# Kernel optimization log

Hardware: AMD Instinct MI355X
Metric: run time of the kernel (lower is better)

Reference implementation:

```python
import jax, jax.numpy as jnp
import numpy as np

B, S, D, H = 2, 2048, 512, 8
HID = 512
DH = HID // H  # 64


def setup_inputs() -> dict:
    key = jax.random.key(0)
    ks = jax.random.split(key, 11)
    sc = 0.02
    return {
        "q": jax.random.normal(ks[0], (B, S, D), jnp.float32),
        "k": jax.random.normal(ks[1], (B, S, D), jnp.float32),
        "v": jax.random.normal(ks[2], (B, S, D), jnp.float32),
        "Wq": jax.random.normal(ks[3], (D, HID), jnp.float32) * sc,
        "bq": jnp.zeros((HID,), jnp.float32),
        "Wk": jax.random.normal(ks[4], (D, HID), jnp.float32) * sc,
        "bk": jnp.zeros((HID,), jnp.float32),
        "Wv": jax.random.normal(ks[5], (D, HID), jnp.float32) * sc,
        "bv": jnp.zeros((HID,), jnp.float32),
        "Wo": jax.random.normal(ks[6], (HID, D), jnp.float32) * sc,
        "bo": jnp.zeros((D,), jnp.float32),
    }


def reference(q, k, v, Wq, bq, Wk, bk, Wv, bv, Wo, bo):
    # Linear projections: [B,S,D] -> [B,S,HID]
    qp = q @ Wq + bq
    kp = k @ Wk + bk
    vp = v @ Wv + bv
    # Faithful to torch .view(B, -1, S, head_dim): raw reshape, NOT a
    # [B,S,H,d] transpose. Head i reads a contiguous block of the buffer.
    qh = qp.reshape(B, H, S, DH)
    kh = kp.reshape(B, H, S, DH)
    vh = vp.reshape(B, H, S, DH)
    # scores [B,H,S,S]; NOTE: original divides by sqrt(d) AFTER softmax.
    scores = jnp.einsum("bhsd,bhtd->bhst", qh, kh)
    attn = jax.nn.softmax(scores, axis=-1) / np.sqrt(DH).astype(np.float32)
    ctx = jnp.einsum("bhst,bhtd->bhsd", attn, vh)
    # torch.cat over heads along last dim -> [B,S,H*d] with head blocks
    concat = jnp.transpose(ctx, (0, 2, 1, 3)).reshape(B, S, HID)
    return concat @ Wo + bo
```

## Files before the change

### kernel.cpp

```cpp
#include <hip/hip_runtime.h>
#include <hip/hip_bf16.h>

typedef __bf16 bf16_t;
typedef __bf16 bf16x8 __attribute__((ext_vector_type(8)));
typedef __bf16 bf16x4 __attribute__((ext_vector_type(4)));
typedef short short4v __attribute__((ext_vector_type(4)));
typedef float f32x4 __attribute__((ext_vector_type(4)));

static_assert(sizeof(bf16x8) == 16, "bf16x8 must be 16B");

#define BB 2
#define SS 2048
#define DD 512
#define HH 8
#define DH 64
#define LOG2E 1.44269504088896f

__global__ void prep(const float* __restrict__ q, const float* __restrict__ k,
                     const float* __restrict__ v, const float* __restrict__ w0,
                     const float* __restrict__ w1, const float* __restrict__ w2,
                     const float* __restrict__ w3, bf16_t* __restrict__ qkvb,
                     bf16_t* __restrict__ wt, int n) {
  const int tid = threadIdx.x;
  if (blockIdx.z < 3) {
    const float* src = (blockIdx.z == 0) ? q : (blockIdx.z == 1) ? k : v;
    bf16_t* out = qkvb + (size_t)blockIdx.z * n;
    int i = (blockIdx.x * 256 + tid) * 8;
    if (i >= n) return;
    const float4* s4 = (const float4*)(src + i);
    float4 a = s4[0], b = s4[1];
    bf16x8 o;
    o[0] = (bf16_t)a.x; o[1] = (bf16_t)a.y; o[2] = (bf16_t)a.z; o[3] = (bf16_t)a.w;
    o[4] = (bf16_t)b.x; o[5] = (bf16_t)b.y; o[6] = (bf16_t)b.z; o[7] = (bf16_t)b.w;
    *(bf16x8*)(out + i) = o;
  } else {
    __shared__ float tile[32][33];
    const int x = blockIdx.x;
    const int wsel = x >> 8;
    const int nb = ((x >> 4) & 15) * 32, kb = (x & 15) * 32;
    const int tx = tid & 31, ty = tid >> 5;
    const float* W = (wsel == 0) ? w0 : (wsel == 1) ? w1 : (wsel == 2) ? w2 : w3;
    bf16_t* out = wt + (size_t)wsel * 512 * 512;
#pragma unroll
    for (int i = 0; i < 4; i++)
      tile[ty + i * 8][tx] = W[(size_t)(kb + ty + i * 8) * 512 + nb + tx];
    __syncthreads();
#pragma unroll
    for (int i = 0; i < 4; i++)
      out[(size_t)(nb + ty + i * 8) * 512 + kb + tx] = (bf16_t)tile[tx][ty + i * 8];
  }
}

template <int BM, int BN, int WM, int WN, typename OutT>
__global__ __launch_bounds__(256) void gemm2(
    const bf16_t* __restrict__ Abase, const bf16_t* __restrict__ Btbase,
    const float* __restrict__ bias0, const float* __restrict__ bias1,
    const float* __restrict__ bias2, OutT* __restrict__ Cbase,
    int M, int N, int K, long Az, long Bz, long Cz, float scale0) {
  static_assert(BM == 2 * WM && BN == 2 * WN, "2x2 wave grid");
  constexpr int FM = WM / 16, FN = WN / 16;
  constexpr int AJ = BM / 32, BJ = BN / 32;

  const bf16_t* A  = Abase + (size_t)blockIdx.z * Az;
  const bf16_t* Bt = Btbase + (size_t)blockIdx.z * Bz;
  const float* bias = (blockIdx.z == 0) ? bias0 : (blockIdx.z == 1) ? bias1 : bias2;
  OutT* C = Cbase + (size_t)blockIdx.z * Cz;
  const float osc = (blockIdx.z == 0) ? scale0 : 1.0f;

  __shared__ bf16_t As[2][BM * 64];
  __shared__ bf16_t Bs[2][BN * 64];

  const int tid = threadIdx.x, w = tid >> 6, l = tid & 63;
  const int bm = blockIdx.y, bn = blockIdx.x;
  const int wm0 = (w >> 1) * WM, wn0 = (w & 1) * WN;
  const int lr = l & 15, lg = l >> 4;

  f32x4 acc[FM][FN] = {};

  auto stage = [&](int buf, int kt) {
#pragma unroll
    for (int j = 0; j < AJ; j++) {
      int lin = j * 256 + tid;
      int row = lin >> 3, cc = lin & 7;
      const bf16_t* g = A + (size_t)(bm * BM + row) * K + kt * 64 + cc * 8;
      __builtin_amdgcn_global_load_lds(
          (const __attribute__((address_space(1))) void*)g,
          (__attribute__((address_space(3))) void*)(&As[buf][(j * 256 + w * 64) * 8]), 16, 0, 0);
    }
#pragma unroll
    for (int j = 0; j < BJ; j++) {
      int lin = j * 256 + tid;
      int row = lin >> 3, cc = lin & 7;
      const bf16_t* g = Bt + (size_t)(bn * BN + row) * K + kt * 64 + cc * 8;
      __builtin_amdgcn_global_load_lds(
          (const __attribute__((address_space(1))) void*)g,
          (__attribute__((address_space(3))) void*)(&Bs[buf][(j * 256 + w * 64) * 8]), 16, 0, 0);
    }
  };

  stage(0, 0);
  const int KT = K >> 6;
  for (int kt = 0; kt < KT; kt++) {
    __syncthreads();
    if (kt + 1 < KT) stage((kt + 1) & 1, kt + 1);
    const bf16_t* as = As[kt & 1];
    const bf16_t* bs = Bs[kt & 1];
#pragma unroll
    for (int kc = 0; kc < 2; kc++) {
      bf16x8 a[FM], b[FN];
#pragma unroll
      for (int i = 0; i < FM; i++)
        a[i] = *(const bf16x8*)(as + (wm0 + i * 16 + lr) * 64 + kc * 32 + lg * 8);
#pragma unroll
      for (int j = 0; j < FN; j++)
        b[j] = *(const bf16x8*)(bs + (wn0 + j * 16 + lr) * 64 + kc * 32 + lg * 8);
#pragma unroll
      for (int i = 0; i < FM; i++)
#pragma unroll
        for (int j = 0; j < FN; j++)
          acc[i][j] = __builtin_amdgcn_mfma_f32_16x16x32_bf16(a[i], b[j], acc[i][j], 0, 0, 0);
    }
  }

  const int row0 = bm * BM + wm0, col0 = bn * BN + wn0;
#pragma unroll
  for (int j = 0; j < FN; j++) {
    int col = col0 + j * 16 + lr;
    float bv = bias[col];
#pragma unroll
    for (int i = 0; i < FM; i++) {
      int row = row0 + i * 16 + lg * 4;
#pragma unroll
      for (int r = 0; r < 4; r++) {
        float vv = (acc[i][j][r] + bv) * osc;
        C[(size_t)(row + r) * N + col] = (OutT)vv;
      }
    }
  }
}

__global__ __launch_bounds__(256, 8) void attn_flash(const bf16_t* __restrict__ qp,
                                                     const bf16_t* __restrict__ kp,
                                                     const bf16_t* __restrict__ vp,
                                                     bf16_t* __restrict__ Opart,
                                                     float* __restrict__ mlpart) {
  const int id = blockIdx.x;
  const int bh = (id & 7) | (((id >> 3) & 1) << 3);
  const int qt = (id >> 4) & 31;
  const int quarter = id >> 9;
  const int pidx = (((qt << 4) | bh) << 2) + quarter;

  const int tid = threadIdx.x, w = tid >> 6, l = tid & 63;
  const int lr = l & 15, lg = l >> 4;
  const size_t hb = (size_t)bh * (SS * DH);
  const bf16_t* Q = qp + hb;
  const bf16_t* Kh = kp + hb;
  const bf16_t* Vh = vp + hb;

  __shared__ __align__(16) bf16_t KsL[2][2048];
  __shared__ __align__(16) bf16_t VtL[2][2048];

  const int qr0 = qt * 64 + w * 16;

  bf16x8 aq[2];
#pragma unroll
  for (int kc = 0; kc < 2; kc++)
    aq[kc] = *(const bf16x8*)(Q + (size_t)(qr0 + lr) * DH + kc * 32 + lg * 8);

  f32x4 o[4] = {};
  float m_run = -1e30f, l_run = 0.f;

  const int krow = (w << 3) + (l >> 3);
  const int kcol = ((l & 7) ^ (l >> 3)) << 3;
  const bf16_t* ks_it = Kh + (size_t)(quarter * 16) * 2048 + krow * 64 + kcol;

  auto stage_k = [&](int buf, const bf16_t* ks) {
    char* kb = (char*)&KsL[buf][0];
    __builtin_amdgcn_global_load_lds((const __attribute__((address_space(1))) void*)ks,
        (__attribute__((address_space(3))) void*)(kb + (w << 10)), 16, 0, 0);
  };

  const int vkv = l & 31;
  const int vdv = (w << 1) | (l >> 5);
  bf16x8 vreg;
  auto load_v = [&](int it) {
    vreg = *(const bf16x8*)(Vh + ((size_t)it * 32 + vkv) * DH + vdv * 8);
  };
  auto write_v = [&](int buf) {
    char* vt = (char*)&VtL[buf][0];
#pragma unroll
    for (int j = 0; j < 8; j++) {
      int d = vdv * 8 + j;
      *(bf16_t*)(vt + d * 64 + ((vkv << 1) ^ (j << 3))) = vreg[j];
    }
  };

  const int it0 = quarter * 16;
  stage_k(0, ks_it);
  load_v(it0);
  write_v(0);

  for (int i = 0; i < 16; i++) {
    const int buf = i & 1;
    __syncthreads();
    if (i + 1 < 16) {
      ks_it += 2048;
      stage_k(buf ^ 1, ks_it);
      load_v(it0 + i + 1);
    }

    const char* ksb = (const char*)&KsL[buf][0];
    f32x4 s[2] = {};
    __builtin_amdgcn_s_setprio(1);
#pragma unroll
    for (int kc = 0; kc < 2; kc++) {
#pragma unroll
      for (int n = 0; n < 2; n++) {
        bf16x8 bk = *(const bf16x8*)(ksb + (n * 16 + lr) * 128 +
                                     ((kc * 64 + lg * 16) ^ ((lr & 7) << 4)));
        s[n] = __builtin_amdgcn_mfma_f32_16x16x32_bf16(bk, aq[kc], s[n], 0, 0, 0);
      }
    }
    __builtin_amdgcn_s_setprio(0);

    float pmax = -1e30f;
#pragma unroll
    for (int n = 0; n < 2; n++)
#pragma unroll
      for (int r = 0; r < 4; r++) pmax = fmaxf(pmax, s[n][r]);
    pmax = fmaxf(pmax, __shfl_xor(pmax, 16));
    pmax = fmaxf(pmax, __shfl_xor(pmax, 32));
    if (!__all(pmax <= m_run + 8.0f)) {
      float mnew = fmaxf(m_run, pmax);
      float scale = exp2f(m_run - mnew);
      l_run *= scale;
#pragma unroll
      for (int n = 0; n < 4; n++)
#pragma unroll
        for (int r = 0; r < 4; r++) o[n][r] *= scale;
      m_run = mnew;
    }
    float rs = 0.f;
#pragma unroll
    for (int n = 0; n < 2; n++)
#pragma unroll
      for (int r = 0; r < 4; r++) {
        float e = exp2f(s[n][r] - m_run);
        s[n][r] = e;
        rs += e;
      }
    l_run += rs;

    short4v pb[2];
#pragma unroll
    for (int c2 = 0; c2 < 2; c2++) {
      bf16x4 t;
#pragma unroll
      for (int r = 0; r < 4; r++) t[r] = (bf16_t)s[c2][r];
      pb[c2] = __builtin_bit_cast(short4v, t);
    }
    const char* vtb = (const char*)&VtL[buf][0];
    __builtin_amdgcn_s_setprio(1);
#pragma unroll
    for (int nd = 0; nd < 4; nd++) {
#pragma unroll
      for (int c2 = 0; c2 < 2; c2++) {
        bf16x4 bvh = *(const bf16x4*)(vtb + (nd * 16 + lr) * 64 +
                                      ((c2 * 32 + lg * 8) ^ ((lr & 7) << 3)));
        o[nd] = __builtin_amdgcn_mfma_f32_16x16x16bf16_1k(
            __builtin_bit_cast(short4v, bvh), pb[c2], o[nd], 0, 0, 0);
      }
    }
    __builtin_amdgcn_s_setprio(0);

    if (i + 1 < 16) write_v(buf ^ 1);
  }

  l_run += __shfl_xor(l_run, 16);
  l_run += __shfl_xor(l_run, 32);

  bf16_t* ob = Opart + (size_t)pidx * 4096;
#pragma unroll
  for (int n = 0; n < 4; n++) {
    bf16x4 t;
#pragma unroll
    for (int r = 0; r < 4; r++) t[r] = (bf16_t)o[n][r];
    *(bf16x4*)(ob + ((w * 4 + n) * 64 + l) * 4) = t;
  }
  if (lg == 0) {
    mlpart[(size_t)pidx * 128 + (w * 16 + lr) * 2 + 0] = m_run;
    mlpart[(size_t)pidx * 128 + (w * 16 + lr) * 2 + 1] = l_run;
  }
}

__global__ __launch_bounds__(256) void attn_combine(const bf16_t* __restrict__ Opart,
                                                    const float* __restrict__ mlpart,
                                                    bf16_t* __restrict__ ctx) {
  const int gid = blockIdx.x;
  const int qt = gid >> 4, bh = gid & 15;
  const int t = threadIdx.x, w = t >> 6, l = t & 63;
  const int lr = l & 15, lg = l >> 4;
  const int q = w * 16 + lr;

  float mv[4], lv[4];
#pragma unroll
  for (int s = 0; s < 4; s++) {
    const float* ml = mlpart + (size_t)(gid * 4 + s) * 128 + q * 2;
    mv[s] = ml[0];
    lv[s] = ml[1];
  }
  float m = fmaxf(fmaxf(mv[0], mv[1]), fmaxf(mv[2], mv[3]));
  float e[4], denom = 0.f;
#pragma unroll
  for (int s = 0; s < 4; s++) { e[s] = exp2f(mv[s] - m); denom += lv[s] * e[s]; }
  denom *= 8.0f;
  float f[4];
#pragma unroll
  for (int s = 0; s < 4; s++) f[s] = e[s] / denom;

  const int b = bh >> 3, h = bh & 7;
  const int trow = qt * 64 + q;
  size_t rowbase = ((size_t)b * SS + trow) * 512 + h * 64;

#pragma unroll
  for (int n = 0; n < 4; n++) {
    float acc[4] = {0.f, 0.f, 0.f, 0.f};
#pragma unroll
    for (int s = 0; s < 4; s++) {
      bf16x4 v = *(const bf16x4*)(Opart + (size_t)(gid * 4 + s) * 4096 +
                                  ((w * 4 + n) * 64 + l) * 4);
#pragma unroll
      for (int r = 0; r < 4; r++) acc[r] += (float)v[r] * f[s];
    }
    bf16x4 ov;
#pragma unroll
    for (int r = 0; r < 4; r++) ov[r] = (bf16_t)acc[r];
    *(bf16x4*)(&ctx[rowbase + n * 16 + lg * 4]) = ov;
  }
}

extern "C" void kernel_launch(void* const* d_in, const int* in_sizes, int n_in,
                              void* d_out, int out_size, void* d_ws, size_t ws_size,
                              hipStream_t stream) {
  const float* q  = (const float*)d_in[0];
  const float* k  = (const float*)d_in[1];
  const float* v  = (const float*)d_in[2];
  const float* Wq = (const float*)d_in[3];
  const float* bq = (const float*)d_in[4];
  const float* Wk = (const float*)d_in[5];
  const float* bk = (const float*)d_in[6];
  const float* Wv = (const float*)d_in[7];
  const float* bv = (const float*)d_in[8];
  const float* Wo = (const float*)d_in[9];
  const float* bo = (const float*)d_in[10];

  const size_t NQKV = (size_t)4096 * 512;
  const size_t NW = (size_t)512 * 512;

  bf16_t* ws   = (bf16_t*)d_ws;
  bf16_t* wt   = ws;
  bf16_t* proj = wt + 4 * NW;
  bf16_t* ctx  = proj + 3 * NQKV;
  bf16_t* qkvb = ctx + NQKV;
  bf16_t* Opart = qkvb;
  float* mlpart = (float*)(Opart + (size_t)2048 * 4096);

  prep<<<dim3(1024, 1, 4), 256, 0, stream>>>(q, k, v, Wq, Wk, Wv, Wo, qkvb, wt, (int)NQKV);
  gemm2<128, 64, 64, 32, bf16_t><<<dim3(8, 32, 3), 256, 0, stream>>>(
      qkvb, wt, bq, bk, bv, proj, 4096, 512, 512, (long)NQKV, (long)NW, (long)NQKV, LOG2E);
  attn_flash<<<2048, 256, 0, stream>>>(proj, proj + NQKV, proj + 2 * NQKV, Opart, mlpart);
  attn_combine<<<512, 256, 0, stream>>>(Opart, mlpart, ctx);
  gemm2<64, 64, 32, 32, float><<<dim3(8, 64, 1), 256, 0, stream>>>(
      ctx, wt + 3 * NW, bo, bo, bo, (float*)d_out, 4096, 512, 512, 0, 0, 0, 1.0f);
}
```

Before: 91.14 us.

## Fuse fp32-to-bf16 activation conversion into QKV projection GEMM staging

Removes the separate pass that converted q/k/v to bf16. The QKV GEMM now loads fp32 activations straight into registers, converts them, and writes them to LDS after the MFMA work of the current tile. This is meant to save the extra global write and read of the bf16 activation copies and one launch's worth of work. In exchange it uses more registers and replaces the asynchronous global-to-LDS loads for A with register-staged loads, which are twice as many bytes per element.

```diff
diff --git a/kernel.cpp b/kernel.cpp
--- a/kernel.cpp
+++ b/kernel.cpp
@@ -16,52 +16,36 @@
 #define DH 64
 #define LOG2E 1.44269504088896f
 
-__global__ void prep(const float* __restrict__ q, const float* __restrict__ k,
-                     const float* __restrict__ v, const float* __restrict__ w0,
-                     const float* __restrict__ w1, const float* __restrict__ w2,
-                     const float* __restrict__ w3, bf16_t* __restrict__ qkvb,
-                     bf16_t* __restrict__ wt, int n) {
-  const int tid = threadIdx.x;
-  if (blockIdx.z < 3) {
-    const float* src = (blockIdx.z == 0) ? q : (blockIdx.z == 1) ? k : v;
-    bf16_t* out = qkvb + (size_t)blockIdx.z * n;
-    int i = (blockIdx.x * 256 + tid) * 8;
-    if (i >= n) return;
-    const float4* s4 = (const float4*)(src + i);
-    float4 a = s4[0], b = s4[1];
-    bf16x8 o;
-    o[0] = (bf16_t)a.x; o[1] = (bf16_t)a.y; o[2] = (bf16_t)a.z; o[3] = (bf16_t)a.w;
-    o[4] = (bf16_t)b.x; o[5] = (bf16_t)b.y; o[6] = (bf16_t)b.z; o[7] = (bf16_t)b.w;
-    *(bf16x8*)(out + i) = o;
-  } else {
-    __shared__ float tile[32][33];
-    const int x = blockIdx.x;
-    const int wsel = x >> 8;
-    const int nb = ((x >> 4) & 15) * 32, kb = (x & 15) * 32;
-    const int tx = tid & 31, ty = tid >> 5;
-    const float* W = (wsel == 0) ? w0 : (wsel == 1) ? w1 : (wsel == 2) ? w2 : w3;
-    bf16_t* out = wt + (size_t)wsel * 512 * 512;
-#pragma unroll
-    for (int i = 0; i < 4; i++)
-      tile[ty + i * 8][tx] = W[(size_t)(kb + ty + i * 8) * 512 + nb + tx];
-    __syncthreads();
-#pragma unroll
-    for (int i = 0; i < 4; i++)
-      out[(size_t)(nb + ty + i * 8) * 512 + kb + tx] = (bf16_t)tile[tx][ty + i * 8];
-  }
+__global__ void transpose_w(const float* __restrict__ w0, const float* __restrict__ w1,
+                            const float* __restrict__ w2, const float* __restrict__ w3,
+                            bf16_t* __restrict__ wt) {
+  __shared__ float tile[32][33];
+  const float* W = (blockIdx.z == 0) ? w0 : (blockIdx.z == 1) ? w1 : (blockIdx.z == 2) ? w2 : w3;
+  bf16_t* out = wt + (size_t)blockIdx.z * 512 * 512;
+  int tx = threadIdx.x, ty = threadIdx.y;
+  int nb = blockIdx.x * 32, kb = blockIdx.y * 32;
+#pragma unroll
+  for (int i = 0; i < 4; i++)
+    tile[ty + i * 8][tx] = W[(size_t)(kb + ty + i * 8) * 512 + nb + tx];
+  __syncthreads();
+#pragma unroll
+  for (int i = 0; i < 4; i++)
+    out[(size_t)(nb + ty + i * 8) * 512 + kb + tx] = (bf16_t)tile[tx][ty + i * 8];
 }
 
-template <int BM, int BN, int WM, int WN, typename OutT>
+template <int BM, int BN, int WM, int WN, int AF32, typename OutT>
 __global__ __launch_bounds__(256) void gemm2(
-    const bf16_t* __restrict__ Abase, const bf16_t* __restrict__ Btbase,
+    const bf16_t* __restrict__ Abf, const float* __restrict__ a0,
+    const float* __restrict__ a1, const float* __restrict__ a2,
+    const bf16_t* __restrict__ Btbase,
     const float* __restrict__ bias0, const float* __restrict__ bias1,
     const float* __restrict__ bias2, OutT* __restrict__ Cbase,
-    int M, int N, int K, long Az, long Bz, long Cz, float scale0) {
+    int M, int N, int K, long Bz, long Cz, float scale0) {
   static_assert(BM == 2 * WM && BN == 2 * WN, "2x2 wave grid");
   constexpr int FM = WM / 16, FN = WN / 16;
   constexpr int AJ = BM / 32, BJ = BN / 32;
 
-  const bf16_t* A  = Abase + (size_t)blockIdx.z * Az;
+  const float* Af = (blockIdx.z == 0) ? a0 : (blockIdx.z == 1) ? a1 : a2;
   const bf16_t* Bt = Btbase + (size_t)blockIdx.z * Bz;
   const float* bias = (blockIdx.z == 0) ? bias0 : (blockIdx.z == 1) ? bias1 : bias2;
   OutT* C = Cbase + (size_t)blockIdx.z * Cz;
@@ -76,17 +60,49 @@
   const int lr = l & 15, lg = l >> 4;
 
   f32x4 acc[FM][FN] = {};
-
-  auto stage = [&](int buf, int kt) {
-#pragma unroll
-    for (int j = 0; j < AJ; j++) {
-      int lin = j * 256 + tid;
-      int row = lin >> 3, cc = lin & 7;
-      const bf16_t* g = A + (size_t)(bm * BM + row) * K + kt * 64 + cc * 8;
-      __builtin_amdgcn_global_load_lds(
-          (const __attribute__((address_space(1))) void*)g,
-          (__attribute__((address_space(3))) void*)(&As[buf][(j * 256 + w * 64) * 8]), 16, 0, 0);
-    }
+  float4 areg[AF32 ? 2 * AJ : 1][AF32 ? 1 : 1];
+  float4 ar[2 * (AF32 ? AJ : 1)];
+
+  auto load_a = [&](int kt) {
+    if constexpr (AF32) {
+#pragma unroll
+      for (int j = 0; j < AJ; j++) {
+        int lin = j * 256 + tid;
+        int row = lin >> 3, cc = lin & 7;
+        const float* g = Af + (size_t)(bm * BM + row) * K + kt * 64 + cc * 8;
+        ar[j * 2 + 0] = *(const float4*)(g);
+        ar[j * 2 + 1] = *(const float4*)(g + 4);
+      }
+    }
+  };
+  auto write_a = [&](int buf) {
+    if constexpr (AF32) {
+#pragma unroll
+      for (int j = 0; j < AJ; j++) {
+        int lin = j * 256 + tid;
+        bf16x8 o;
+        o[0] = (bf16_t)ar[j * 2 + 0].x; o[1] = (bf16_t)ar[j * 2 + 0].y;
+        o[2] = (bf16_t)ar[j * 2 + 0].z; o[3] = (bf16_t)ar[j * 2 + 0].w;
+        o[4] = (bf16_t)ar[j * 2 + 1].x; o[5] = (bf16_t)ar[j * 2 + 1].y;
+        o[6] = (bf16_t)ar[j * 2 + 1].z; o[7] = (bf16_t)ar[j * 2 + 1].w;
+        *(bf16x8*)(&As[buf][lin * 8]) = o;
+      }
+    }
+  };
+  auto stage_a_bf = [&](int buf, int kt) {
+    if constexpr (!AF32) {
+#pragma unroll
+      for (int j = 0; j < AJ; j++) {
+        int lin = j * 256 + tid;
+        int row = lin >> 3, cc = lin & 7;
+        const bf16_t* g = Abf + (size_t)(bm * BM + row) * K + kt * 64 + cc * 8;
+        __builtin_amdgcn_global_load_lds(
+            (const __attribute__((address_space(1))) void*)g,
+            (__attribute__((address_space(3))) void*)(&As[buf][(j * 256 + w * 64) * 8]), 16, 0, 0);
+      }
+    }
+  };
+  auto stage_b = [&](int buf, int kt) {
 #pragma unroll
     for (int j = 0; j < BJ; j++) {
       int lin = j * 256 + tid;
@@ -98,11 +114,19 @@
     }
   };
 
-  stage(0, 0);
+  load_a(0);
+  stage_b(0, 0);
+  stage_a_bf(0, 0);
+  write_a(0);
+
   const int KT = K >> 6;
   for (int kt = 0; kt < KT; kt++) {
     __syncthreads();
-    if (kt + 1 < KT) stage((kt + 1) & 1, kt + 1);
+    if (kt + 1 < KT) {
+      load_a(kt + 1);
+      stage_b((kt + 1) & 1, kt + 1);
+      stage_a_bf((kt + 1) & 1, kt + 1);
+    }
     const bf16_t* as = As[kt & 1];
     const bf16_t* bs = Bs[kt & 1];
 #pragma unroll
@@ -120,6 +144,7 @@
         for (int j = 0; j < FN; j++)
           acc[i][j] = __builtin_amdgcn_mfma_f32_16x16x32_bf16(a[i], b[j], acc[i][j], 0, 0, 0);
     }
+    if (kt + 1 < KT) write_a((kt + 1) & 1);
   }
 
   const int row0 = bm * BM + wm0, col0 = bn * BN + wn0;
@@ -361,15 +386,15 @@
   bf16_t* wt   = ws;
   bf16_t* proj = wt + 4 * NW;
   bf16_t* ctx  = proj + 3 * NQKV;
-  bf16_t* qkvb = ctx + NQKV;
-  bf16_t* Opart = qkvb;
+  bf16_t* Opart = ctx + NQKV;
   float* mlpart = (float*)(Opart + (size_t)2048 * 4096);
 
-  prep<<<dim3(1024, 1, 4), 256, 0, stream>>>(q, k, v, Wq, Wk, Wv, Wo, qkvb, wt, (int)NQKV);
-  gemm2<128, 64, 64, 32, bf16_t><<<dim3(8, 32, 3), 256, 0, stream>>>(
-      qkvb, wt, bq, bk, bv, proj, 4096, 512, 512, (long)NQKV, (long)NW, (long)NQKV, LOG2E);
+  transpose_w<<<dim3(16, 16, 4), dim3(32, 8), 0, stream>>>(Wq, Wk, Wv, Wo, wt);
+  gemm2<128, 64, 64, 32, 1, bf16_t><<<dim3(8, 32, 3), 256, 0, stream>>>(
+      nullptr, q, k, v, wt, bq, bk, bv, proj, 4096, 512, 512, (long)NW, (long)NQKV, LOG2E);
   attn_flash<<<2048, 256, 0, stream>>>(proj, proj + NQKV, proj + 2 * NQKV, Opart, mlpart);
   attn_combine<<<512, 256, 0, stream>>>(Opart, mlpart, ctx);
-  gemm2<64, 64, 32, 32, float><<<dim3(8, 64, 1), 256, 0, stream>>>(
-      ctx, wt + 3 * NW, bo, bo, bo, (float*)d_out, 4096, 512, 512, 0, 0, 0, 1.0f);
+  gemm2<64, 64, 32, 32, 0, float><<<dim3(8, 64, 1), 256, 0, stream>>>(
+      ctx, nullptr, nullptr, nullptr, wt + 3 * NW, bo, bo, bo, (float*)d_out,
+      4096, 512, 512, 0, 0, 1.0f);
 }
```

Result: slower. 99.44 us (+9.1%).

## Process two KV tiles per barrier with four-deep LDS buffering in attention

Applied to the files above, without the earlier changes.

The flash-attention loop now stages two K/V tiles per iteration into a 4-slot LDS ring and computes both tiles between barriers, which halves the number of __syncthreads and deepens prefetch. Shared memory per block doubles to 32 KB and launch bounds drop from 8 to 4 blocks per CU, and keeping two V register sets live raises register pressure. The cost is lower possible occupancy in exchange for fewer synchronisations and more loads in flight.

```diff
diff --git a/kernel.cpp b/kernel.cpp
--- a/kernel.cpp
+++ b/kernel.cpp
@@ -139,7 +139,7 @@
   }
 }
 
-__global__ __launch_bounds__(256, 8) void attn_flash(const bf16_t* __restrict__ qp,
+__global__ __launch_bounds__(256, 4) void attn_flash(const bf16_t* __restrict__ qp,
                                                      const bf16_t* __restrict__ kp,
                                                      const bf16_t* __restrict__ vp,
                                                      bf16_t* __restrict__ Opart,
@@ -157,8 +157,8 @@
   const bf16_t* Kh = kp + hb;
   const bf16_t* Vh = vp + hb;
 
-  __shared__ __align__(16) bf16_t KsL[2][2048];
-  __shared__ __align__(16) bf16_t VtL[2][2048];
+  __shared__ __align__(16) bf16_t KsL[4][2048];
+  __shared__ __align__(16) bf16_t VtL[4][2048];
 
   const int qr0 = qt * 64 + w * 16;
 
@@ -182,33 +182,31 @@
 
   const int vkv = l & 31;
   const int vdv = (w << 1) | (l >> 5);
-  bf16x8 vreg;
-  auto load_v = [&](int it) {
-    vreg = *(const bf16x8*)(Vh + ((size_t)it * 32 + vkv) * DH + vdv * 8);
-  };
-  auto write_v = [&](int buf) {
+  bf16x8 vregA, vregB;
+  auto load_vA = [&](int it) {
+    vregA = *(const bf16x8*)(Vh + ((size_t)it * 32 + vkv) * DH + vdv * 8);
+  };
+  auto load_vB = [&](int it) {
+    vregB = *(const bf16x8*)(Vh + ((size_t)it * 32 + vkv) * DH + vdv * 8);
+  };
+  auto write_vA = [&](int buf) {
     char* vt = (char*)&VtL[buf][0];
 #pragma unroll
     for (int j = 0; j < 8; j++) {
       int d = vdv * 8 + j;
-      *(bf16_t*)(vt + d * 64 + ((vkv << 1) ^ (j << 3))) = vreg[j];
-    }
-  };
-
-  const int it0 = quarter * 16;
-  stage_k(0, ks_it);
-  load_v(it0);
-  write_v(0);
-
-  for (int i = 0; i < 16; i++) {
-    const int buf = i & 1;
-    __syncthreads();
-    if (i + 1 < 16) {
-      ks_it += 2048;
-      stage_k(buf ^ 1, ks_it);
-      load_v(it0 + i + 1);
-    }
-
+      *(bf16_t*)(vt + d * 64 + ((vkv << 1) ^ (j << 3))) = vregA[j];
+    }
+  };
+  auto write_vB = [&](int buf) {
+    char* vt = (char*)&VtL[buf][0];
+#pragma unroll
+    for (int j = 0; j < 8; j++) {
+      int d = vdv * 8 + j;
+      *(bf16_t*)(vt + d * 64 + ((vkv << 1) ^ (j << 3))) = vregB[j];
+    }
+  };
+
+  auto tile_body = [&](int buf) {
     const char* ksb = (const char*)&KsL[buf][0];
     f32x4 s[2] = {};
     __builtin_amdgcn_s_setprio(1);
@@ -272,8 +270,34 @@
       }
     }
     __builtin_amdgcn_s_setprio(0);
-
-    if (i + 1 < 16) write_v(buf ^ 1);
+  };
+
+  const int it0 = quarter * 16;
+  stage_k(0, ks_it);
+  stage_k(1, ks_it + 2048);
+  load_vA(it0);
+  load_vB(it0 + 1);
+  write_vA(0);
+  write_vB(1);
+
+  for (int i = 0; i < 8; i++) {
+    const int ta = 2 * i;
+    __syncthreads();
+    if (i + 1 < 8) {
+      ks_it += 4096;
+      stage_k((ta + 2) & 3, ks_it);
+      stage_k((ta + 3) & 3, ks_it + 2048);
+      load_vA(it0 + ta + 2);
+      load_vB(it0 + ta + 3);
+    }
+
+    tile_body(ta & 3);
+    tile_body((ta + 1) & 3);
+
+    if (i + 1 < 8) {
+      write_vA((ta + 2) & 3);
+      write_vB((ta + 3) & 3);
+    }
   }
 
   l_run += __shfl_xor(l_run, 16);
```

Measured after the change: 92.02 us. About the same (+1.0%).
